# Kernel tuning notes

Measured on AMD Instinct MI355X. Metric: run time of the kernel, lower is better.

The kernel has to match this reference:

```python
import jax, jax.numpy as jnp
import numpy as np

N_NODES = 100000
D = 128


def gcn_conv(x, W, b, src, dst, deg_inv_sqrt):
    # PyG GCNConv: linear transform, symmetric-normalized aggregation with self-loops, bias
    h = x @ W  # [N, D_out]
    norm = deg_inv_sqrt[src] * deg_inv_sqrt[dst]  # [E_tot]
    msgs = h[src] * norm[:, None]  # gather + scale  [E_tot, D_out]
    out = jax.ops.segment_sum(msgs, dst, num_segments=x.shape[0])  # scatter-add to targets
    return out + b


def _prep_edges(edge_index, n_nodes):
    # add self-loops (weight 1) and compute deg^{-1/2} over targets (flow source_to_target)
    loops = jnp.arange(n_nodes, dtype=edge_index.dtype)
    src = jnp.concatenate([edge_index[0], loops])
    dst = jnp.concatenate([edge_index[1], loops])
    deg = jax.ops.segment_sum(jnp.ones_like(dst, dtype=jnp.float32), dst, num_segments=n_nodes)
    deg_inv_sqrt = jnp.where(deg > 0, jax.lax.rsqrt(jnp.maximum(deg, 1.0)), 0.0)
    return src, dst, deg_inv_sqrt


def setup_inputs() -> dict:
    key = jax.random.key(0)
    ks = jax.random.split(key, 8)
    node_fts = jax.random.normal(ks[0], (N_NODES, D), dtype=jnp.float32)
    edge_index = jax.random.randint(ks[1], (2, 1600000), 0, N_NODES, dtype=jnp.int64)
    scale = 1.0 / np.sqrt(D)
    W1 = jax.random.uniform(ks[2], (D, D), jnp.float32, -scale, scale)
    b1 = jnp.zeros((D,), jnp.float32)
    W2 = jax.random.uniform(ks[3], (D, D), jnp.float32, -scale, scale)
    b2 = jnp.zeros((D,), jnp.float32)
    W3 = jax.random.uniform(ks[4], (D, D), jnp.float32, -scale, scale)
    b3 = jnp.zeros((D,), jnp.float32)
    return {"node_fts": node_fts, "edge_index": edge_index,
            "W1": W1, "b1": b1, "W2": W2, "b2": b2, "W3": W3, "b3": b3}


def reference(node_fts, edge_index, W1, b1, W2, b2, W3, b3):
    n = node_fts.shape[0]
    src, dst, dinv = _prep_edges(edge_index, n)
    x = jax.nn.relu(gcn_conv(node_fts, W1, b1, src, dst, dinv))
    x = jax.nn.relu(gcn_conv(x, W2, b2, src, dst, dinv))
    x = jax.nn.relu(gcn_conv(x, W3, b3, src, dst, dinv))
    return x
```

## Files before the change

### kernel.cpp

```cpp
#include <hip/hip_runtime.h>

#define NN 100000
#define EE 1600000
#define D 128
#define NPART 8
#define PSZ (NN / NPART)
#define NI4 (EE / 4)
#define SUBW 196
#define NSB (NPART * 64)
#define SCAP 4096
#define RCAP 8192
#define LBCAP 96

typedef __attribute__((ext_vector_type(8))) short bf16x8;
typedef __attribute__((ext_vector_type(4))) float f32x4;

__device__ inline unsigned int f2bf2(float a, float b) {
    unsigned int ua = __float_as_uint(a);
    unsigned int ub = __float_as_uint(b);
    ua = (ua + 0x7fffu + ((ua >> 16) & 1u)) >> 16;
    ub = (ub + 0x7fffu + ((ub >> 16) & 1u)) >> 16;
    return ua | (ub << 16);
}
__device__ inline unsigned short f2bf(float a) {
    unsigned int u = __float_as_uint(a);
    return (unsigned short)((u + 0x7fffu + ((u >> 16) & 1u)) >> 16);
}
__device__ inline float2 bf2f2(unsigned int u) {
    return make_float2(__uint_as_float(u << 16), __uint_as_float(u & 0xffff0000u));
}


__global__ __launch_bounds__(256) void fbwt_kernel(const int4* __restrict__ src4,
                                                   const int4* __restrict__ dst4,
                                                   int* __restrict__ gcur2,
                                                   uint2* __restrict__ buckets2,
                                                   int* __restrict__ deg,
                                                   const float* __restrict__ W1,
                                                   const float* __restrict__ W2,
                                                   const float* __restrict__ W3,
                                                   unsigned short* __restrict__ wt1,
                                                   unsigned short* __restrict__ wt2,
                                                   unsigned short* __restrict__ wt3,
                                                   unsigned int* __restrict__ hb) {
    if (blockIdx.x >= 512) {
        const int g = (blockIdx.x - 512) * 256 + threadIdx.x;
        const int n = g >> 7, k = g & 127;
        wt1[n * 128 + k] = f2bf(W1[k * 128 + n]);
        wt2[n * 128 + k] = f2bf(W2[k * 128 + n]);
        wt3[n * 128 + k] = f2bf(W3[k * 128 + n]);
        if (blockIdx.x == 512 && threadIdx.x < 64) hb[(size_t)NN * 64 + threadIdx.x] = 0;
        return;
    }
    __shared__ uint2 bins[64][LBCAP];
    __shared__ int bcnt[64];
    __shared__ int gbase[64];
    const int p = blockIdx.x >> 6;
    const int c = blockIdx.x & 63;
    if (threadIdx.x < 64) bcnt[threadIdx.x] = 0;
    __syncthreads();
    const int lo = p * PSZ, hi = lo + PSZ;
    const int chunk4 = NI4 / 64;
    const int a0 = c * chunk4, a1 = a0 + chunk4;
    for (int i = a0 + threadIdx.x; i < a1; i += 256) {
        int4 d4 = dst4[i];
        bool m0 = (d4.x >= lo && d4.x < hi);
        bool m1 = (d4.y >= lo && d4.y < hi);
        bool m2 = (d4.z >= lo && d4.z < hi);
        bool m3 = (d4.w >= lo && d4.w < hi);
        if (!(m0 | m1 | m2 | m3)) continue;
        int4 s4 = src4[i];
        int ss[4] = {s4.x, s4.y, s4.z, s4.w};
        int dd[4] = {d4.x, d4.y, d4.z, d4.w};
        bool mm[4] = {m0, m1, m2, m3};
#pragma unroll
        for (int k = 0; k < 4; ++k) {
            if (!mm[k]) continue;
            atomicAdd(&deg[dd[k]], 1);
            int li = (dd[k] - lo) / SUBW;
            int pos = atomicAdd(&bcnt[li], 1);
            if (pos < LBCAP) {
                bins[li][pos] = make_uint2((unsigned)ss[k], (unsigned)dd[k]);
            } else {
                int sb = p * 64 + li;
                int gp = atomicAdd(&gcur2[sb], 1);
                buckets2[(size_t)sb * SCAP + gp] = make_uint2((unsigned)ss[k], (unsigned)dd[k]);
            }
        }
    }
    __syncthreads();
    if (threadIdx.x < 64) {
        int cc = min(bcnt[threadIdx.x], LBCAP);
        gbase[threadIdx.x] = atomicAdd(&gcur2[p * 64 + threadIdx.x], cc);
        bcnt[threadIdx.x] = cc;
    }
    __syncthreads();
    for (int b = 0; b < 64; ++b) {
        const int cc = bcnt[b];
        uint2* outp = buckets2 + (size_t)(p * 64 + b) * SCAP + gbase[b];
        for (int i = threadIdx.x; i < cc; i += 256) outp[i] = bins[b][i];
    }
}


template <bool F32IN>
__device__ __forceinline__ void gemm_body(int wave, const void* __restrict__ xin,
                                          const unsigned short* __restrict__ wt,
                                          const int* __restrict__ deg,
                                          unsigned int* __restrict__ hb) {
    const int base = wave * 64;
    if (base >= NN) return;
    const int lane = threadIdx.x & 63;
    const int r = lane & 15;
    const int q = lane >> 4;
    const unsigned short* wrow = wt + (size_t)r * 128 + q * 8;
    bf16x8 wfr[4][8];
#pragma unroll
    for (int kc = 0; kc < 4; ++kc)
#pragma unroll
        for (int nt = 0; nt < 8; ++nt)
            wfr[kc][nt] = *(const bf16x8*)(wrow + (size_t)nt * 16 * 128 + kc * 32);
#pragma unroll
    for (int tt = 0; tt < 4; ++tt) {
        const int m0 = base + tt * 16;
        if (m0 >= NN) break;
        f32x4 acc[8] = {};
#pragma unroll
        for (int kc = 0; kc < 4; ++kc) {
            bf16x8 xf;
            if (F32IN) {
                const float* xrow = (const float*)xin + (size_t)(m0 + r) * 128 + q * 8 + kc * 32;
                float4 a = *(const float4*)xrow;
                float4 b = *(const float4*)(xrow + 4);
                unsigned short tmp[8] = {f2bf(a.x), f2bf(a.y), f2bf(a.z), f2bf(a.w),
                                         f2bf(b.x), f2bf(b.y), f2bf(b.z), f2bf(b.w)};
                xf = *(const bf16x8*)tmp;
            } else {
                const unsigned short* xrow =
                    (const unsigned short*)xin + (size_t)(m0 + r) * 128 + q * 8 + kc * 32;
                xf = *(const bf16x8*)xrow;
            }
#pragma unroll
            for (int nt = 0; nt < 8; ++nt)
                acc[nt] = __builtin_amdgcn_mfma_f32_16x16x32_bf16(wfr[kc][nt], xf, acc[nt], 0, 0, 0);
        }
        const int orow = m0 + r;
        const float dvr = rsqrtf(1.0f + (float)deg[orow]);
        unsigned int* hrow = hb + (size_t)orow * 64;
#pragma unroll
        for (int nt = 0; nt < 8; ++nt) {
            int n = nt * 16 + q * 4;
            *(uint2*)(hrow + (n >> 1)) =
                make_uint2(f2bf2(acc[nt][0] * dvr, acc[nt][1] * dvr),
                           f2bf2(acc[nt][2] * dvr, acc[nt][3] * dvr));
        }
    }
}


__global__ __launch_bounds__(256, 2) void sort3_gemm1_kernel(const uint2* __restrict__ buckets2,
                                                             const int* __restrict__ gcur2,
                                                             int* __restrict__ csr,
                                                             int* __restrict__ info,
                                                             float* __restrict__ dinv,
                                                             const float* __restrict__ x0,
                                                             const unsigned short* __restrict__ wt1,
                                                             const int* __restrict__ deg,
                                                             unsigned int* __restrict__ hb) {
    __shared__ int hist[256];
    __shared__ int pscan[256];
    __shared__ int lcur[256];
    __shared__ int staged[RCAP];
    if (blockIdx.x >= 512) {
        const int wave = (blockIdx.x - 512) * 4 + (threadIdx.x >> 6);
        gemm_body<true>(wave, (const void*)x0, wt1, deg, hb);
        return;
    }
    const int sb = blockIdx.x;
    const int li = sb & 63;
    const int base_node = (sb >> 6) * PSZ + li * SUBW;
    const int nnodes = min(SUBW, PSZ - li * SUBW);
    const int scnt = gcur2[sb];
    const uint2* bk = buckets2 + (size_t)sb * SCAP;
    const int t = threadIdx.x;
    hist[t] = 0;
    __syncthreads();
    for (int i = t; i < scnt; i += 256) atomicAdd(&hist[(int)bk[i].y - base_node], 1);
    __syncthreads();
    const int padded = (t < nnodes) ? ((hist[t] + 7) & ~7) : 0;
    pscan[t] = padded;
    __syncthreads();
    for (int off = 1; off < 256; off <<= 1) {
        int v = (t >= off) ? pscan[t - off] : 0;
        __syncthreads();
        pscan[t] += v;
        __syncthreads();
    }
    const int rstart = pscan[t] - padded;
    lcur[t] = rstart;
    __syncthreads();
    const int total = pscan[255];
    for (int i = t; i < total; i += 256) staged[i] = NN;
    __syncthreads();
    for (int i = t; i < scnt; i += 256) {
        uint2 r = bk[i];
        int pos = atomicAdd(&lcur[(int)r.y - base_node], 1);
        staged[pos] = (int)r.x;
    }
    __syncthreads();
    int4* co = (int4*)(csr + (size_t)sb * RCAP);
    for (int i = t; i < (total >> 2); i += 256) co[i] = ((const int4*)staged)[i];
    if (t < nnodes) {
        int dg = hist[t];
        info[base_node + t] = ((sb * RCAP + rstart) << 8) | dg;
        dinv[base_node + t] = rsqrtf(1.0f + (float)dg);
    }
}

template <bool F32IN>
__global__ __launch_bounds__(256, 2) void gemm_kernel(const void* __restrict__ xin,
                                                      const unsigned short* __restrict__ wt,
                                                      const int* __restrict__ deg,
                                                      unsigned int* __restrict__ hb) {
    const int wave = blockIdx.x * 4 + (threadIdx.x >> 6);
    gemm_body<F32IN>(wave, xin, wt, deg, hb);
}


template <bool BF16OUT>
__global__ __launch_bounds__(256) void aggregate_kernel(const unsigned int* __restrict__ hb,
                                                        const int* __restrict__ csr,
                                                        const int* __restrict__ info,
                                                        const float* __restrict__ dinv,
                                                        const float2* __restrict__ bias2,
                                                        void* __restrict__ outp) {
    const int d = blockIdx.x * 4 + (threadIdx.x >> 6);
    const int j = threadIdx.x & 63;
    const int ifo = info[d];
    int e = ifo >> 8;
    const int end = e + (((ifo & 255) + 7) & ~7);
    float2 acc = bf2f2(hb[(size_t)d * 64 + j]);
    for (; e + 16 <= end; e += 16) {
        int4 c0 = *(const int4*)(csr + e);
        int4 c1 = *(const int4*)(csr + e + 4);
        int4 c2 = *(const int4*)(csr + e + 8);
        int4 c3 = *(const int4*)(csr + e + 12);
        unsigned int v0 = hb[(size_t)c0.x * 64 + j];
        unsigned int v1 = hb[(size_t)c0.y * 64 + j];
        unsigned int v2 = hb[(size_t)c0.z * 64 + j];
        unsigned int v3 = hb[(size_t)c0.w * 64 + j];
        unsigned int v4 = hb[(size_t)c1.x * 64 + j];
        unsigned int v5 = hb[(size_t)c1.y * 64 + j];
        unsigned int v6 = hb[(size_t)c1.z * 64 + j];
        unsigned int v7 = hb[(size_t)c1.w * 64 + j];
        unsigned int v8 = hb[(size_t)c2.x * 64 + j];
        unsigned int v9 = hb[(size_t)c2.y * 64 + j];
        unsigned int va = hb[(size_t)c2.z * 64 + j];
        unsigned int vb = hb[(size_t)c2.w * 64 + j];
        unsigned int vc = hb[(size_t)c3.x * 64 + j];
        unsigned int vd = hb[(size_t)c3.y * 64 + j];
        unsigned int ve = hb[(size_t)c3.z * 64 + j];
        unsigned int vf = hb[(size_t)c3.w * 64 + j];
        float2 f0 = bf2f2(v0), f1 = bf2f2(v1), f2 = bf2f2(v2), f3 = bf2f2(v3);
        float2 f4 = bf2f2(v4), f5 = bf2f2(v5), f6 = bf2f2(v6), f7 = bf2f2(v7);
        float2 f8 = bf2f2(v8), f9 = bf2f2(v9), fa = bf2f2(va), fb = bf2f2(vb);
        float2 fc = bf2f2(vc), fd = bf2f2(vd), fe = bf2f2(ve), ff = bf2f2(vf);
        acc.x += ((f0.x + f1.x) + (f2.x + f3.x)) + ((f4.x + f5.x) + (f6.x + f7.x)) +
                 ((f8.x + f9.x) + (fa.x + fb.x)) + ((fc.x + fd.x) + (fe.x + ff.x));
        acc.y += ((f0.y + f1.y) + (f2.y + f3.y)) + ((f4.y + f5.y) + (f6.y + f7.y)) +
                 ((f8.y + f9.y) + (fa.y + fb.y)) + ((fc.y + fd.y) + (fe.y + ff.y));
    }
    if (e < end) {
        int4 c0 = *(const int4*)(csr + e);
        int4 c1 = *(const int4*)(csr + e + 4);
        unsigned int v0 = hb[(size_t)c0.x * 64 + j];
        unsigned int v1 = hb[(size_t)c0.y * 64 + j];
        unsigned int v2 = hb[(size_t)c0.z * 64 + j];
        unsigned int v3 = hb[(size_t)c0.w * 64 + j];
        unsigned int v4 = hb[(size_t)c1.x * 64 + j];
        unsigned int v5 = hb[(size_t)c1.y * 64 + j];
        unsigned int v6 = hb[(size_t)c1.z * 64 + j];
        unsigned int v7 = hb[(size_t)c1.w * 64 + j];
        float2 f0 = bf2f2(v0), f1 = bf2f2(v1), f2 = bf2f2(v2), f3 = bf2f2(v3);
        float2 f4 = bf2f2(v4), f5 = bf2f2(v5), f6 = bf2f2(v6), f7 = bf2f2(v7);
        acc.x += ((f0.x + f1.x) + (f2.x + f3.x)) + ((f4.x + f5.x) + (f6.x + f7.x));
        acc.y += ((f0.y + f1.y) + (f2.y + f3.y)) + ((f4.y + f5.y) + (f6.y + f7.y));
    }
    const float dv = dinv[d];
    float2 bb = bias2[j];
    float ox = fmaxf(dv * acc.x + bb.x, 0.0f);
    float oy = fmaxf(dv * acc.y + bb.y, 0.0f);
    if (BF16OUT) {
        ((unsigned int*)outp)[(size_t)d * 64 + j] = f2bf2(ox, oy);
    } else {
        ((float2*)outp)[(size_t)d * 64 + j] = make_float2(ox, oy);
    }
}


extern "C" void kernel_launch(void* const* d_in, const int* in_sizes, int n_in,
                              void* d_out, int out_size, void* d_ws, size_t ws_size,
                              hipStream_t stream) {
    const float* x0 = (const float*)d_in[0];
    const int* ei = (const int*)d_in[1];
    const float* W1 = (const float*)d_in[2];
    const float* b1 = (const float*)d_in[3];
    const float* W2 = (const float*)d_in[4];
    const float* b2 = (const float*)d_in[5];
    const float* W3 = (const float*)d_in[6];
    const float* b3 = (const float*)d_in[7];
    float* out = (float*)d_out;

    char* ws = (char*)d_ws;
    size_t off = 0;
    auto alloc = [&](size_t bytes) -> void* {
        off = (off + 511) & ~(size_t)511;
        void* p = ws + off;
        off += bytes;
        return p;
    };
    unsigned int* hb  = (unsigned int*)alloc(((size_t)NN + 1) * 64 * 4);
    int*   csr     = (int*)  alloc((size_t)NSB * RCAP * sizeof(int));
    uint2* buckets2 = (uint2*)alloc((size_t)NSB * SCAP * sizeof(uint2));
    int*   info    = (int*)  alloc((size_t)NN * sizeof(int));
    float* dinv    = (float*)alloc((size_t)NN * sizeof(float));
    int*   deg     = (int*)  alloc((size_t)NN * sizeof(int));
    int*   gcur2   = (int*)  alloc(NSB * sizeof(int));
    unsigned short* wt1 = (unsigned short*)alloc(128 * 128 * 2);
    unsigned short* wt2 = (unsigned short*)alloc(128 * 128 * 2);
    unsigned short* wt3 = (unsigned short*)alloc(128 * 128 * 2);

    unsigned int* xact = (unsigned int*)d_out;

    const int4* src4 = (const int4*)ei;
    const int4* dst4 = (const int4*)(ei + EE);

    hipMemsetAsync(gcur2, 0, NSB * sizeof(int), stream);
    hipMemsetAsync(deg, 0, (size_t)NN * sizeof(int), stream);
    fbwt_kernel<<<576, 256, 0, stream>>>(src4, dst4, gcur2, buckets2, deg,
                                         W1, W2, W3, wt1, wt2, wt3, hb);
    sort3_gemm1_kernel<<<903, 256, 0, stream>>>(buckets2, gcur2, csr, info, dinv,
                                                x0, wt1, deg, hb);
    aggregate_kernel<true><<<NN / 4, 256, 0, stream>>>(hb, csr, info, dinv,
                                                       (const float2*)b1, (void*)xact);
    gemm_kernel<false><<<391, 256, 0, stream>>>((const void*)xact, wt2, deg, hb);
    aggregate_kernel<true><<<NN / 4, 256, 0, stream>>>(hb, csr, info, dinv,
                                                       (const float2*)b2, (void*)xact);
    gemm_kernel<false><<<391, 256, 0, stream>>>((const void*)xact, wt3, deg, hb);
    aggregate_kernel<false><<<NN / 4, 256, 0, stream>>>(hb, csr, info, dinv,
                                                        (const float2*)b3, (void*)out);
}
```

Before: 436.5 us.

## Split degree counting into dedicated blocks, tile weight transpose, persistent aggregation grid

The first kernel now counts degrees in separate blocks that scan all destination indices, instead of doing it inside the per-partition binning loops. Binning uses twice as many chunks per partition with a smaller local bin capacity. The weight transpose goes through a shared-memory tile so global reads and writes are coalesced. The aggregation kernels switch from one-wave-per-node launches to a fixed 2048-block grid-stride loop. Together these aim to spread the edge-bucketing work more evenly and cut block launch overhead, at the cost of more global overflow atomics from the smaller local bins.

Measured after the change: 448.9 us. +2.9%, slower.

```diff
diff --git a/kernel.cpp b/kernel.cpp
--- a/kernel.cpp
+++ b/kernel.cpp
@@ -2,7 +2,6 @@
 
 #define NN 100000
 #define EE 1600000
-#define D 128
 #define NPART 8
 #define PSZ (NN / NPART)
 #define NI4 (EE / 4)
@@ -10,7 +9,11 @@
 #define NSB (NPART * 64)
 #define SCAP 4096
 #define RCAP 8192
-#define LBCAP 96
+#define FCHUNKS 128
+#define FBLOCKS (NPART * FCHUNKS)
+#define WTBLOCKS 48
+#define DEGB 64
+#define LBCAP 48
 
 typedef __attribute__((ext_vector_type(8))) short bf16x8;
 typedef __attribute__((ext_vector_type(4))) float f32x4;
@@ -43,25 +46,52 @@
                                                    unsigned short* __restrict__ wt2,
                                                    unsigned short* __restrict__ wt3,
                                                    unsigned int* __restrict__ hb) {
-    if (blockIdx.x >= 512) {
-        const int g = (blockIdx.x - 512) * 256 + threadIdx.x;
-        const int n = g >> 7, k = g & 127;
-        wt1[n * 128 + k] = f2bf(W1[k * 128 + n]);
-        wt2[n * 128 + k] = f2bf(W2[k * 128 + n]);
-        wt3[n * 128 + k] = f2bf(W3[k * 128 + n]);
-        if (blockIdx.x == 512 && threadIdx.x < 64) hb[(size_t)NN * 64 + threadIdx.x] = 0;
-        return;
-    }
     __shared__ uint2 bins[64][LBCAP];
     __shared__ int bcnt[64];
     __shared__ int gbase[64];
-    const int p = blockIdx.x >> 6;
-    const int c = blockIdx.x & 63;
+    __shared__ float tile[32][33];
+    const int bx = blockIdx.x;
+
+    if (bx < DEGB) {
+        const int a0 = bx * (NI4 / DEGB);
+        const int a1 = a0 + (NI4 / DEGB);
+        for (int i = a0 + threadIdx.x; i < a1; i += 256) {
+            int4 d4 = dst4[i];
+            atomicAdd(&deg[d4.x], 1);
+            atomicAdd(&deg[d4.y], 1);
+            atomicAdd(&deg[d4.z], 1);
+            atomicAdd(&deg[d4.w], 1);
+        }
+        return;
+    }
+
+    if (bx < DEGB + WTBLOCKS) {
+        const int wb = bx - DEGB;
+        const int m = wb >> 4;
+        const int tl = wb & 15;
+        const int ti = tl >> 2, tj = tl & 3;
+        const float* W = m == 0 ? W1 : (m == 1 ? W2 : W3);
+        unsigned short* wt = m == 0 ? wt1 : (m == 1 ? wt2 : wt3);
+        const int r = threadIdx.x >> 5, c = threadIdx.x & 31;
+#pragma unroll
+        for (int rr = r; rr < 32; rr += 8)
+            tile[rr][c] = W[(ti * 32 + rr) * 128 + tj * 32 + c];
+        __syncthreads();
+#pragma unroll
+        for (int rr = r; rr < 32; rr += 8)
+            wt[(size_t)(tj * 32 + rr) * 128 + ti * 32 + c] = f2bf(tile[c][rr]);
+        if (wb == 0 && threadIdx.x < 64) hb[(size_t)NN * 64 + threadIdx.x] = 0;
+        return;
+    }
+
+    const int fb = bx - DEGB - WTBLOCKS;
+    const int p = fb >> 7;
+    const int ch = fb & 127;
     if (threadIdx.x < 64) bcnt[threadIdx.x] = 0;
     __syncthreads();
     const int lo = p * PSZ, hi = lo + PSZ;
-    const int chunk4 = NI4 / 64;
-    const int a0 = c * chunk4, a1 = a0 + chunk4;
+    const int chunk4 = NI4 / FCHUNKS;
+    const int a0 = ch * chunk4, a1 = a0 + chunk4;
     for (int i = a0 + threadIdx.x; i < a1; i += 256) {
         int4 d4 = dst4[i];
         bool m0 = (d4.x >= lo && d4.x < hi);
@@ -76,7 +106,6 @@
 #pragma unroll
         for (int k = 0; k < 4; ++k) {
             if (!mm[k]) continue;
-            atomicAdd(&deg[dd[k]], 1);
             int li = (dd[k] - lo) / SUBW;
             int pos = atomicAdd(&bcnt[li], 1);
             if (pos < LBCAP) {
@@ -228,13 +257,12 @@
 
 
 template <bool BF16OUT>
-__global__ __launch_bounds__(256) void aggregate_kernel(const unsigned int* __restrict__ hb,
-                                                        const int* __restrict__ csr,
-                                                        const int* __restrict__ info,
-                                                        const float* __restrict__ dinv,
-                                                        const float2* __restrict__ bias2,
-                                                        void* __restrict__ outp) {
-    const int d = blockIdx.x * 4 + (threadIdx.x >> 6);
+__device__ __forceinline__ void agg_node(int d, const unsigned int* __restrict__ hb,
+                                         const int* __restrict__ csr,
+                                         const int* __restrict__ info,
+                                         const float* __restrict__ dinv,
+                                         const float2* __restrict__ bias2,
+                                         void* __restrict__ outp) {
     const int j = threadIdx.x & 63;
     const int ifo = info[d];
     int e = ifo >> 8;
@@ -297,6 +325,19 @@
     }
 }
 
+template <bool BF16OUT>
+__global__ __launch_bounds__(256) void aggregate_kernel(const unsigned int* __restrict__ hb,
+                                                        const int* __restrict__ csr,
+                                                        const int* __restrict__ info,
+                                                        const float* __restrict__ dinv,
+                                                        const float2* __restrict__ bias2,
+                                                        void* __restrict__ outp) {
+    const int w = threadIdx.x >> 6;
+    const int stride = (int)gridDim.x * 4;
+    for (int d = blockIdx.x * 4 + w; d < NN; d += stride)
+        agg_node<BF16OUT>(d, hb, csr, info, dinv, bias2, outp);
+}
+
 
 extern "C" void kernel_launch(void* const* d_in, const int* in_sizes, int n_in,
                               void* d_out, int out_size, void* d_ws, size_t ws_size,
@@ -337,16 +378,16 @@
 
     hipMemsetAsync(gcur2, 0, NSB * sizeof(int), stream);
     hipMemsetAsync(deg, 0, (size_t)NN * sizeof(int), stream);
-    fbwt_kernel<<<576, 256, 0, stream>>>(src4, dst4, gcur2, buckets2, deg,
-                                         W1, W2, W3, wt1, wt2, wt3, hb);
+    fbwt_kernel<<<DEGB + WTBLOCKS + FBLOCKS, 256, 0, stream>>>(src4, dst4, gcur2, buckets2, deg,
+                                                               W1, W2, W3, wt1, wt2, wt3, hb);
     sort3_gemm1_kernel<<<903, 256, 0, stream>>>(buckets2, gcur2, csr, info, dinv,
                                                 x0, wt1, deg, hb);
-    aggregate_kernel<true><<<NN / 4, 256, 0, stream>>>(hb, csr, info, dinv,
-                                                       (const float2*)b1, (void*)xact);
+    aggregate_kernel<true><<<2048, 256, 0, stream>>>(hb, csr, info, dinv,
+                                                     (const float2*)b1, (void*)xact);
     gemm_kernel<false><<<391, 256, 0, stream>>>((const void*)xact, wt2, deg, hb);
-    aggregate_kernel<true><<<NN / 4, 256, 0, stream>>>(hb, csr, info, dinv,
-                                                       (const float2*)b2, (void*)xact);
+    aggregate_kernel<true><<<2048, 256, 0, stream>>>(hb, csr, info, dinv,
+                                                     (const float2*)b2, (void*)xact);
     gemm_kernel<false><<<391, 256, 0, stream>>>((const void*)xact, wt3, deg, hb);
-    aggregate_kernel<false><<<NN / 4, 256, 0, stream>>>(hb, csr, info, dinv,
-                                                        (const float2*)b3, (void*)out);
-}
+    aggregate_kernel<false><<<2048, 256, 0, stream>>>(hb, csr, info, dinv,
+                                                      (const float2*)b3, (void*)out);
+}
```
